# Kernel optimization log

Hardware: AMD Instinct MI355X
Metric: run time of the kernel (lower is better)

Reference implementation:

```python
import jax, jax.numpy as jnp
import numpy as np

B, C, D, O = 262144, 256, 64, 8


def setup_inputs() -> dict:
    key = jax.random.key(0)
    k1, k2, k3, k4 = jax.random.split(key, 4)
    inputs = jax.random.normal(k1, (B, D), dtype=jnp.float32)
    cluster_centers = jax.random.normal(k2, (C, D), dtype=jnp.float32)
    # widths initialized ~ N(1.0, 0.05) as in the layer
    widths = 1.0 + 0.05 * jax.random.normal(k3, (C,), dtype=jnp.float32)
    # rule_weights ~ N(0, 0.05)
    rule_weights = 0.05 * jax.random.normal(k4, (C, O), dtype=jnp.float32)
    return {"inputs": inputs, "cluster_centers": cluster_centers,
            "widths": widths, "rule_weights": rule_weights}


def reference(inputs, cluster_centers, widths, rule_weights):
    # Squared L2 distances via ||a-c||^2 = ||a||^2 + ||c||^2 - 2 a.c
    # (avoids materializing the [B, C, D] broadcast diff tensor)
    x_sq = jnp.sum(inputs * inputs, axis=1, keepdims=True)          # [B, 1]
    c_sq = jnp.sum(cluster_centers * cluster_centers, axis=1)       # [C]
    cross = inputs @ cluster_centers.T                               # [B, C]
    dists_squared = x_sq + c_sq[None, :] - 2.0 * cross               # [B, C]
    # Gaussian membership with per-cluster widths
    memb = jnp.exp(-dists_squared / (2.0 * widths * widths))         # [B, C]
    # Normalize over clusters (sum-normalization, not softmax-of-logits)
    memb_norm = memb / jnp.sum(memb, axis=1, keepdims=True)          # [B, C]
    # Weighted rule consequents
    return memb_norm @ rule_weights                                  # [B, O]
```

## Files before the change

### kernel.cpp

```cpp
#include <hip/hip_runtime.h>


#define NB 262144
#define NC 256
#define ND 64
#define NO 8

typedef __attribute__((ext_vector_type(8))) short short8;
typedef __attribute__((ext_vector_type(8))) _Float16 half8;
typedef __attribute__((ext_vector_type(16))) float floatx16;

#define WOFF 20480
#define WS_SHORTS 28672

__device__ inline unsigned short f2bf(float f) {
    unsigned u = __builtin_bit_cast(unsigned, f);
    u = u + 0x7FFFu + ((u >> 16) & 1u);
    return (unsigned short)(u >> 16);
}

struct Raw8 { float4 r0, r1, r2, r3, r4, r5, r6, r7; };
struct XF { half8 k0, k1, k2, k3, f12; };

__device__ __forceinline__ Raw8 load_x(const float* __restrict__ xrow, int h) {
    const float4* xp = (const float4*)xrow;
    Raw8 r;
    r.r0 = xp[0 + 2 * h];  r.r1 = xp[1 + 2 * h];
    r.r2 = xp[4 + 2 * h];  r.r3 = xp[5 + 2 * h];
    r.r4 = xp[8 + 2 * h];  r.r5 = xp[9 + 2 * h];
    r.r6 = xp[12 + 2 * h]; r.r7 = xp[13 + 2 * h];
    return r;
}

__device__ __forceinline__ half8 cvt8(float4 a, float4 b, float& part) {
    float v[8] = {a.x, a.y, a.z, a.w, b.x, b.y, b.z, b.w};
    half8 hh;
#pragma unroll
    for (int j = 0; j < 8; ++j) {
        part = fmaf(v[j], v[j], part);
        hh[j] = (_Float16)v[j];
    }
    return hh;
}

__device__ __forceinline__ XF convert_x(const Raw8& r, int h) {
    float part = 0.0f;
    XF f;
    f.k0 = cvt8(r.r0, r.r1, part);
    f.k1 = cvt8(r.r2, r.r3, part);
    f.k2 = cvt8(r.r4, r.r5, part);
    f.k3 = cvt8(r.r6, r.r7, part);
    float xsq = part + __shfl_xor(part, 32, 64);
    float sh = (float)(_Float16)xsq;
    float sl = xsq - sh;
    half8 ff;
#pragma unroll
    for (int j = 0; j < 8; ++j) ff[j] = (_Float16)0.0f;
    if (h == 0) {
        ff[0] = (_Float16)sh;
        ff[1] = (_Float16)sl;
        ff[2] = (_Float16)sh;
        ff[3] = (_Float16)1.0f;
        ff[4] = (_Float16)1.0f;
    }
    f.f12 = ff;
    return f;
}

__device__ __forceinline__ void compute_btile(const short* lds_s, int lane, int h,
                                              const XF& xf, float* __restrict__ outp) {
    floatx16 acc2;
#pragma unroll
    for (int i = 0; i < 16; ++i) acc2[i] = 0.0f;

#pragma unroll 1
    for (int t = 0; t < 8; ++t) {
        const half8 A0 = *(const half8*)&lds_s[((t * 5 + 0) * 64 + lane) * 8];
        const half8 A1 = *(const half8*)&lds_s[((t * 5 + 1) * 64 + lane) * 8];
        const half8 A2 = *(const half8*)&lds_s[((t * 5 + 2) * 64 + lane) * 8];
        const half8 A3 = *(const half8*)&lds_s[((t * 5 + 3) * 64 + lane) * 8];
        const half8 C12 = *(const half8*)&lds_s[((t * 5 + 4) * 64 + lane) * 8];
        const short8 w0 = *(const short8*)&lds_s[WOFF + ((2 * t + 0) * 64 + lane) * 8];
        const short8 w1 = *(const short8*)&lds_s[WOFF + ((2 * t + 1) * 64 + lane) * 8];

        floatx16 acc;
#pragma unroll
        for (int i = 0; i < 16; ++i) acc[i] = 0.0f;
        acc = __builtin_amdgcn_mfma_f32_32x32x16_f16(A0, xf.k0, acc, 0, 0, 0);
        acc = __builtin_amdgcn_mfma_f32_32x32x16_f16(A1, xf.k1, acc, 0, 0, 0);
        acc = __builtin_amdgcn_mfma_f32_32x32x16_f16(A2, xf.k2, acc, 0, 0, 0);
        acc = __builtin_amdgcn_mfma_f32_32x32x16_f16(A3, xf.k3, acc, 0, 0, 0);
        acc = __builtin_amdgcn_mfma_f32_32x32x16_f16(C12, xf.f12, acc, 0, 0, 0);

        unsigned p0 = __builtin_bit_cast(unsigned, __builtin_amdgcn_exp2f(acc[0]));
        unsigned p1 = __builtin_bit_cast(unsigned, __builtin_amdgcn_exp2f(acc[1]));
        unsigned p2 = __builtin_bit_cast(unsigned, __builtin_amdgcn_exp2f(acc[2]));
        unsigned p3 = __builtin_bit_cast(unsigned, __builtin_amdgcn_exp2f(acc[3]));
        unsigned p4 = __builtin_bit_cast(unsigned, __builtin_amdgcn_exp2f(acc[4]));
        unsigned p5 = __builtin_bit_cast(unsigned, __builtin_amdgcn_exp2f(acc[5]));
        unsigned p6 = __builtin_bit_cast(unsigned, __builtin_amdgcn_exp2f(acc[6]));
        unsigned p7 = __builtin_bit_cast(unsigned, __builtin_amdgcn_exp2f(acc[7]));
        unsigned p8 = __builtin_bit_cast(unsigned, __builtin_amdgcn_exp2f(acc[8]));
        unsigned p9 = __builtin_bit_cast(unsigned, __builtin_amdgcn_exp2f(acc[9]));
        unsigned pa = __builtin_bit_cast(unsigned, __builtin_amdgcn_exp2f(acc[10]));
        unsigned pb = __builtin_bit_cast(unsigned, __builtin_amdgcn_exp2f(acc[11]));
        unsigned pc = __builtin_bit_cast(unsigned, __builtin_amdgcn_exp2f(acc[12]));
        unsigned pd = __builtin_bit_cast(unsigned, __builtin_amdgcn_exp2f(acc[13]));
        unsigned pe = __builtin_bit_cast(unsigned, __builtin_amdgcn_exp2f(acc[14]));
        unsigned pf = __builtin_bit_cast(unsigned, __builtin_amdgcn_exp2f(acc[15]));
        uint4 q0, q1;
        q0.x = __builtin_amdgcn_perm(p1, p0, 0x07060302u);
        q0.y = __builtin_amdgcn_perm(p3, p2, 0x07060302u);
        q0.z = __builtin_amdgcn_perm(p5, p4, 0x07060302u);
        q0.w = __builtin_amdgcn_perm(p7, p6, 0x07060302u);
        q1.x = __builtin_amdgcn_perm(p9, p8, 0x07060302u);
        q1.y = __builtin_amdgcn_perm(pb, pa, 0x07060302u);
        q1.z = __builtin_amdgcn_perm(pd, pc, 0x07060302u);
        q1.w = __builtin_amdgcn_perm(pf, pe, 0x07060302u);
        short8 pf0 = __builtin_bit_cast(short8, q0);
        short8 pf1 = __builtin_bit_cast(short8, q1);

        acc2 = __builtin_amdgcn_mfma_f32_32x32x16_bf16(w0, pf0, acc2, 0, 0, 0);
        acc2 = __builtin_amdgcn_mfma_f32_32x32x16_bf16(w1, pf1, acc2, 0, 0, 0);
    }

    float S = acc2[4];
    float Sp = __shfl_xor(S, 32, 64);
    if (h) S = Sp;
    float inv = 1.0f / S;
    float4 r;
    r.x = acc2[0] * inv;
    r.y = acc2[1] * inv;
    r.z = acc2[2] * inv;
    r.w = acc2[3] * inv;
    ((float4*)outp)[h] = r;
}

__global__ __launch_bounds__(512, 4) void fuzzy_main(
    const float* __restrict__ x,
    const float* __restrict__ centers,
    const float* __restrict__ widths,
    const float* __restrict__ W,
    float* __restrict__ out) {
    __shared__ short lds_s[WS_SHORTS];

    const int tid = threadIdx.x;
    const int wave = tid >> 6;
    const int lane = tid & 63;
    const int col = lane & 31;
    const int h = lane >> 5;
    const int bbase = (blockIdx.x * 8 + wave) * 64;
    const int b0 = bbase + col;
    const int b1 = bbase + 32 + col;

    Raw8 raw0 = load_x(x + (size_t)b0 * ND, h);

    {
        const int t = wave;
        const int c = 32 * t + ((col & 19) | ((col & 4) << 1) | ((col & 8) >> 1));
        const float* cr = centers + c * ND;
        float vv[4][8];
        float part = 0.0f;
#pragma unroll
        for (int kd = 0; kd < 4; ++kd) {
            const float4* p = (const float4*)(cr + kd * 16 + h * 8);
            float4 a0 = p[0], a1 = p[1];
            vv[kd][0] = a0.x; vv[kd][1] = a0.y; vv[kd][2] = a0.z; vv[kd][3] = a0.w;
            vv[kd][4] = a1.x; vv[kd][5] = a1.y; vv[kd][6] = a1.z; vv[kd][7] = a1.w;
#pragma unroll
            for (int j = 0; j < 8; ++j) part = fmaf(vv[kd][j], vv[kd][j], part);
        }
        float csq = part + __shfl_xor(part, 32, 64);
        float w = widths[c];
        float kk = 1.4426950408889634f / (2.0f * w * w);

#pragma unroll
        for (int kd = 0; kd < 4; ++kd) {
            half8 ah;
#pragma unroll
            for (int j = 0; j < 8; ++j) ah[j] = (_Float16)(2.0f * kk * vv[kd][j]);
            *(half8*)&lds_s[((t * 5 + kd) * 64 + lane) * 8] = ah;
        }
        half8 av;
#pragma unroll
        for (int j = 0; j < 8; ++j) av[j] = (_Float16)0.0f;
        if (h == 0) {
            float kh = (float)(_Float16)kk;
            float kl = kk - kh;
            float Bc = csq * kk;
            float Bh = (float)(_Float16)Bc;
            float Bl = Bc - Bh;
            av[0] = (_Float16)(-kh);
            av[1] = (_Float16)(-kh);
            av[2] = (_Float16)(-kl);
            av[3] = (_Float16)(-Bh);
            av[4] = (_Float16)(-Bl);
        }
        *(half8*)&lds_s[((t * 5 + 4) * 64 + lane) * 8] = av;

#pragma unroll
        for (int q = 0; q < 2; ++q) {
            int k2 = 2 * t + q;
            short8 wf;
#pragma unroll
            for (int j = 0; j < 8; ++j) {
                int c2 = k2 * 16 + h * 8 + j;
                float val = (col < NO) ? W[c2 * NO + col] : (col == 8 ? 1.0f : 0.0f);
                wf[j] = (short)f2bf(val);
            }
            *(short8*)&lds_s[WOFF + (k2 * 64 + lane) * 8] = wf;
        }
    }

    Raw8 raw1 = load_x(x + (size_t)b1 * ND, h);

    XF xf0 = convert_x(raw0, h);
    __syncthreads();

    compute_btile(lds_s, lane, h, xf0, out + (size_t)b0 * NO);

    XF xf1 = convert_x(raw1, h);
    compute_btile(lds_s, lane, h, xf1, out + (size_t)b1 * NO);
}

extern "C" void kernel_launch(void* const* d_in, const int* in_sizes, int n_in,
                              void* d_out, int out_size, void* d_ws, size_t ws_size,
                              hipStream_t stream) {
    const float* x       = (const float*)d_in[0];
    const float* centers = (const float*)d_in[1];
    const float* widths  = (const float*)d_in[2];
    const float* W       = (const float*)d_in[3];
    float* out = (float*)d_out;
    (void)d_ws; (void)ws_size;

    fuzzy_main<<<NB / 512, 512, 0, stream>>>(x, centers, widths, W, out);
}
```

Measured before the change: 110.6 us.

## Interleave two batch tiles per loop to share LDS loads and overlap MFMA with exp

Fuses the two sequential per-tile passes into one loop that processes both 32-row batch tiles per cluster chunk. Each LDS fragment of centers and weights is loaded once and used for both tiles, which halves LDS traffic. Interleaving gives the scheduler independent MFMA and exp work to overlap. The second x tile load is also issued before the center setup to hide global latency. The cost is higher register pressure from two live accumulator sets and both converted x tiles, which may hurt the 4-blocks-per-CU occupancy target.

```diff
diff --git a/kernel.cpp b/kernel.cpp
--- a/kernel.cpp
+++ b/kernel.cpp
@@ -67,63 +67,21 @@
     return f;
 }
 
-__device__ __forceinline__ void compute_btile(const short* lds_s, int lane, int h,
-                                              const XF& xf, float* __restrict__ outp) {
-    floatx16 acc2;
-#pragma unroll
-    for (int i = 0; i < 16; ++i) acc2[i] = 0.0f;
-
-#pragma unroll 1
-    for (int t = 0; t < 8; ++t) {
-        const half8 A0 = *(const half8*)&lds_s[((t * 5 + 0) * 64 + lane) * 8];
-        const half8 A1 = *(const half8*)&lds_s[((t * 5 + 1) * 64 + lane) * 8];
-        const half8 A2 = *(const half8*)&lds_s[((t * 5 + 2) * 64 + lane) * 8];
-        const half8 A3 = *(const half8*)&lds_s[((t * 5 + 3) * 64 + lane) * 8];
-        const half8 C12 = *(const half8*)&lds_s[((t * 5 + 4) * 64 + lane) * 8];
-        const short8 w0 = *(const short8*)&lds_s[WOFF + ((2 * t + 0) * 64 + lane) * 8];
-        const short8 w1 = *(const short8*)&lds_s[WOFF + ((2 * t + 1) * 64 + lane) * 8];
-
-        floatx16 acc;
-#pragma unroll
-        for (int i = 0; i < 16; ++i) acc[i] = 0.0f;
-        acc = __builtin_amdgcn_mfma_f32_32x32x16_f16(A0, xf.k0, acc, 0, 0, 0);
-        acc = __builtin_amdgcn_mfma_f32_32x32x16_f16(A1, xf.k1, acc, 0, 0, 0);
-        acc = __builtin_amdgcn_mfma_f32_32x32x16_f16(A2, xf.k2, acc, 0, 0, 0);
-        acc = __builtin_amdgcn_mfma_f32_32x32x16_f16(A3, xf.k3, acc, 0, 0, 0);
-        acc = __builtin_amdgcn_mfma_f32_32x32x16_f16(C12, xf.f12, acc, 0, 0, 0);
-
-        unsigned p0 = __builtin_bit_cast(unsigned, __builtin_amdgcn_exp2f(acc[0]));
-        unsigned p1 = __builtin_bit_cast(unsigned, __builtin_amdgcn_exp2f(acc[1]));
-        unsigned p2 = __builtin_bit_cast(unsigned, __builtin_amdgcn_exp2f(acc[2]));
-        unsigned p3 = __builtin_bit_cast(unsigned, __builtin_amdgcn_exp2f(acc[3]));
-        unsigned p4 = __builtin_bit_cast(unsigned, __builtin_amdgcn_exp2f(acc[4]));
-        unsigned p5 = __builtin_bit_cast(unsigned, __builtin_amdgcn_exp2f(acc[5]));
-        unsigned p6 = __builtin_bit_cast(unsigned, __builtin_amdgcn_exp2f(acc[6]));
-        unsigned p7 = __builtin_bit_cast(unsigned, __builtin_amdgcn_exp2f(acc[7]));
-        unsigned p8 = __builtin_bit_cast(unsigned, __builtin_amdgcn_exp2f(acc[8]));
-        unsigned p9 = __builtin_bit_cast(unsigned, __builtin_amdgcn_exp2f(acc[9]));
-        unsigned pa = __builtin_bit_cast(unsigned, __builtin_amdgcn_exp2f(acc[10]));
-        unsigned pb = __builtin_bit_cast(unsigned, __builtin_amdgcn_exp2f(acc[11]));
-        unsigned pc = __builtin_bit_cast(unsigned, __builtin_amdgcn_exp2f(acc[12]));
-        unsigned pd = __builtin_bit_cast(unsigned, __builtin_amdgcn_exp2f(acc[13]));
-        unsigned pe = __builtin_bit_cast(unsigned, __builtin_amdgcn_exp2f(acc[14]));
-        unsigned pf = __builtin_bit_cast(unsigned, __builtin_amdgcn_exp2f(acc[15]));
-        uint4 q0, q1;
-        q0.x = __builtin_amdgcn_perm(p1, p0, 0x07060302u);
-        q0.y = __builtin_amdgcn_perm(p3, p2, 0x07060302u);
-        q0.z = __builtin_amdgcn_perm(p5, p4, 0x07060302u);
-        q0.w = __builtin_amdgcn_perm(p7, p6, 0x07060302u);
-        q1.x = __builtin_amdgcn_perm(p9, p8, 0x07060302u);
-        q1.y = __builtin_amdgcn_perm(pb, pa, 0x07060302u);
-        q1.z = __builtin_amdgcn_perm(pd, pc, 0x07060302u);
-        q1.w = __builtin_amdgcn_perm(pf, pe, 0x07060302u);
-        short8 pf0 = __builtin_bit_cast(short8, q0);
-        short8 pf1 = __builtin_bit_cast(short8, q1);
-
-        acc2 = __builtin_amdgcn_mfma_f32_32x32x16_bf16(w0, pf0, acc2, 0, 0, 0);
-        acc2 = __builtin_amdgcn_mfma_f32_32x32x16_bf16(w1, pf1, acc2, 0, 0, 0);
-    }
-
+__device__ __forceinline__ void exp_pack(const floatx16& acc, short8& pf0, short8& pf1) {
+    unsigned q[8];
+#pragma unroll
+    for (int i = 0; i < 8; ++i) {
+        unsigned lo = __builtin_bit_cast(unsigned, __builtin_amdgcn_exp2f(acc[2 * i]));
+        unsigned hi = __builtin_bit_cast(unsigned, __builtin_amdgcn_exp2f(acc[2 * i + 1]));
+        q[i] = __builtin_amdgcn_perm(hi, lo, 0x07060302u);
+    }
+    uint4 q0; q0.x = q[0]; q0.y = q[1]; q0.z = q[2]; q0.w = q[3];
+    uint4 q1; q1.x = q[4]; q1.y = q[5]; q1.z = q[6]; q1.w = q[7];
+    pf0 = __builtin_bit_cast(short8, q0);
+    pf1 = __builtin_bit_cast(short8, q1);
+}
+
+__device__ __forceinline__ void finish(const floatx16& acc2, int h, float* __restrict__ outp) {
     float S = acc2[4];
     float Sp = __shfl_xor(S, 32, 64);
     if (h) S = Sp;
@@ -136,6 +94,59 @@
     ((float4*)outp)[h] = r;
 }
 
+__device__ __forceinline__ void compute_pair(const short* lds_s, int lane, int h,
+                                             const XF& xf0, const XF& xf1,
+                                             float* __restrict__ out0,
+                                             float* __restrict__ out1) {
+    floatx16 accA, accB;
+#pragma unroll
+    for (int i = 0; i < 16; ++i) { accA[i] = 0.0f; accB[i] = 0.0f; }
+
+#pragma unroll 1
+    for (int t = 0; t < 8; ++t) {
+        const half8 A0 = *(const half8*)&lds_s[((t * 5 + 0) * 64 + lane) * 8];
+        const half8 A1 = *(const half8*)&lds_s[((t * 5 + 1) * 64 + lane) * 8];
+        const half8 A2 = *(const half8*)&lds_s[((t * 5 + 2) * 64 + lane) * 8];
+        const half8 A3 = *(const half8*)&lds_s[((t * 5 + 3) * 64 + lane) * 8];
+        const half8 C12 = *(const half8*)&lds_s[((t * 5 + 4) * 64 + lane) * 8];
+        const short8 w0 = *(const short8*)&lds_s[WOFF + ((2 * t + 0) * 64 + lane) * 8];
+        const short8 w1 = *(const short8*)&lds_s[WOFF + ((2 * t + 1) * 64 + lane) * 8];
+
+        {
+            floatx16 acc;
+#pragma unroll
+            for (int i = 0; i < 16; ++i) acc[i] = 0.0f;
+            acc = __builtin_amdgcn_mfma_f32_32x32x16_f16(A0, xf0.k0, acc, 0, 0, 0);
+            acc = __builtin_amdgcn_mfma_f32_32x32x16_f16(A1, xf0.k1, acc, 0, 0, 0);
+            acc = __builtin_amdgcn_mfma_f32_32x32x16_f16(A2, xf0.k2, acc, 0, 0, 0);
+            acc = __builtin_amdgcn_mfma_f32_32x32x16_f16(A3, xf0.k3, acc, 0, 0, 0);
+            acc = __builtin_amdgcn_mfma_f32_32x32x16_f16(C12, xf0.f12, acc, 0, 0, 0);
+            short8 pf0, pf1;
+            exp_pack(acc, pf0, pf1);
+            accA = __builtin_amdgcn_mfma_f32_32x32x16_bf16(w0, pf0, accA, 0, 0, 0);
+            accA = __builtin_amdgcn_mfma_f32_32x32x16_bf16(w1, pf1, accA, 0, 0, 0);
+        }
+
+        {
+            floatx16 acc;
+#pragma unroll
+            for (int i = 0; i < 16; ++i) acc[i] = 0.0f;
+            acc = __builtin_amdgcn_mfma_f32_32x32x16_f16(A0, xf1.k0, acc, 0, 0, 0);
+            acc = __builtin_amdgcn_mfma_f32_32x32x16_f16(A1, xf1.k1, acc, 0, 0, 0);
+            acc = __builtin_amdgcn_mfma_f32_32x32x16_f16(A2, xf1.k2, acc, 0, 0, 0);
+            acc = __builtin_amdgcn_mfma_f32_32x32x16_f16(A3, xf1.k3, acc, 0, 0, 0);
+            acc = __builtin_amdgcn_mfma_f32_32x32x16_f16(C12, xf1.f12, acc, 0, 0, 0);
+            short8 pf0, pf1;
+            exp_pack(acc, pf0, pf1);
+            accB = __builtin_amdgcn_mfma_f32_32x32x16_bf16(w0, pf0, accB, 0, 0, 0);
+            accB = __builtin_amdgcn_mfma_f32_32x32x16_bf16(w1, pf1, accB, 0, 0, 0);
+        }
+    }
+
+    finish(accA, h, out0);
+    finish(accB, h, out1);
+}
+
 __global__ __launch_bounds__(512, 4) void fuzzy_main(
     const float* __restrict__ x,
     const float* __restrict__ centers,
@@ -154,6 +165,7 @@
     const int b1 = bbase + 32 + col;
 
     Raw8 raw0 = load_x(x + (size_t)b0 * ND, h);
+    Raw8 raw1 = load_x(x + (size_t)b1 * ND, h);
 
     {
         const int t = wave;
@@ -212,15 +224,12 @@
         }
     }
 
-    Raw8 raw1 = load_x(x + (size_t)b1 * ND, h);
-
     XF xf0 = convert_x(raw0, h);
+    XF xf1 = convert_x(raw1, h);
     __syncthreads();
 
-    compute_btile(lds_s, lane, h, xf0, out + (size_t)b0 * NO);
-
-    XF xf1 = convert_x(raw1, h);
-    compute_btile(lds_s, lane, h, xf1, out + (size_t)b1 * NO);
+    compute_pair(lds_s, lane, h, xf0, xf1,
+                 out + (size_t)b0 * NO, out + (size_t)b1 * NO);
 }
 
 extern "C" void kernel_launch(void* const* d_in, const int* in_sizes, int n_in,
```

Measured after the change: 111.6 us. About the same (+0.9%).
